# Kernel optimization log

Measured on AMD Instinct MI355X. Metric: run time of the kernel, lower is better.

Reference implementation:

```python
import jax, jax.numpy as jnp
import numpy as np

B, N, C = 2, 2048, 1024
H, HD = 16, 64
PX, PY, PS = 24, 24, 16  # S2RoPE head_dim split (px+py+ps == head_dim)


def rotate_half(t):
    t1, t2 = jnp.split(t, 2, axis=-1)
    return jnp.concatenate([-t2, t1], axis=-1)


def apply_phase_rope(t, phase):
    # t: [B, N, H, d_seg] (d_seg even), phase: [B, N, d_seg//2] angles in radians
    ang = jnp.concatenate([phase, phase], axis=-1)[:, :, None, :]  # [B,N,1,d_seg]
    return t * jnp.cos(ang) + rotate_half(t) * jnp.sin(ang)


def s2rope(t, phase_x, phase_y, phase_sph):
    # spherical RoPE: rotate three disjoint segments of head_dim by the
    # per-token x / y / spherical phases
    tx, ty, ts = t[..., :PX], t[..., PX:PX + PY], t[..., PX + PY:]
    return jnp.concatenate([
        apply_phase_rope(tx, phase_x),
        apply_phase_rope(ty, phase_y),
        apply_phase_rope(ts, phase_sph),
    ], axis=-1)


def setup_inputs() -> dict:
    key = jax.random.key(0)
    ks = jax.random.split(key, 9)
    two_pi = 6.2831853
    return {
        "x": jax.random.normal(ks[0], (B, N, C), dtype=jnp.float32),
        "phase_x": jax.random.uniform(ks[1], (B, N, PX // 2), dtype=jnp.float32) * two_pi,
        "phase_y": jax.random.uniform(ks[2], (B, N, PY // 2), dtype=jnp.float32) * two_pi,
        "phase_sph": jax.random.uniform(ks[3], (B, N, PS // 2), dtype=jnp.float32) * two_pi,
        "rope_mask": jax.random.randint(ks[4], (B, N), 0, 2).astype(bool),
        "Wqkv": jax.random.normal(ks[5], (C, 3 * C), dtype=jnp.float32) * (C ** -0.5),
        "bqkv": jax.random.normal(ks[6], (3 * C,), dtype=jnp.float32) * 0.02,
        "Wproj": jax.random.normal(ks[7], (C, C), dtype=jnp.float32) * (C ** -0.5),
        "bproj": jax.random.normal(ks[8], (C,), dtype=jnp.float32) * 0.02,
    }


def reference(x, phase_x, phase_y, phase_sph, rope_mask, Wqkv, bqkv, Wproj, bproj):
    # qkv projection -> [B, N, 3, H, HD]
    qkv = (x @ Wqkv + bqkv).reshape(B, N, 3, H, HD)
    q, k, v = qkv[:, :, 0], qkv[:, :, 1], qkv[:, :, 2]  # each [B, N, H, HD]

    # template path: S2RoPE with rope_mask selecting which tokens are rotated
    q_rope = s2rope(q, phase_x, phase_y, phase_sph)
    k_rope = s2rope(k, phase_x, phase_y, phase_sph)
    m = rope_mask[:, :, None, None]  # [B, N, 1, 1]
    q = jnp.where(m, q_rope, q)
    k = jnp.where(m, k_rope, k)

    scale = HD ** -0.5
    # [B, H, N, N] scores, softmax over keys, then weighted sum of values
    attn = jax.nn.softmax(jnp.einsum('bnhd,bmhd->bhnm', q, k) * scale, axis=-1)
    out = jnp.einsum('bhnm,bmhd->bnhd', attn, v).reshape(B, N, C)
    return out @ Wproj + bproj
```

## Files before the change

### kernel.cpp

```cpp
#include <hip/hip_runtime.h>
#include <hip/hip_fp16.h>

typedef _Float16 f16;
typedef unsigned int u32;
typedef _Float16 f16x4 __attribute__((ext_vector_type(4)));
typedef _Float16 f16x8 __attribute__((ext_vector_type(8)));
typedef float f32x4 __attribute__((ext_vector_type(4)));
typedef float f32x16 __attribute__((ext_vector_type(16)));

#define B_  2
#define N_  2048
#define C_  1024
#define H_  16
#define HD_ 64

__device__ __forceinline__ void gload_lds16(const void* g, void* l) {
  __builtin_amdgcn_global_load_lds((const __attribute__((address_space(1))) u32*)g,
                                   (__attribute__((address_space(3))) u32*)l,
                                   16, 0, 0);
}

__device__ __forceinline__ u32 pack_f16(float a, float b) {
  auto h2 = __builtin_amdgcn_cvt_pkrtz(a, b);
  return __builtin_bit_cast(u32, h2);
}

__global__ void detect_mask(const u32* __restrict__ m, int* __restrict__ flag) {
  __shared__ int bad;
  if (threadIdx.x == 0) bad = 0;
  __syncthreads();
  int v = 0;
  for (int i = threadIdx.x; i < 1024; i += 256) {
    u32 w = m[i];
    if (w != 0u && w != 1u && w != 0x3F800000u) v = 1;
  }
  if (v) atomicOr(&bad, 1);
  __syncthreads();
  if (threadIdx.x == 0) *flag = bad;
}

__global__ __launch_bounds__(256) void cvt_x(const float* __restrict__ in,
                                             f16* __restrict__ out, int n8) {
  const int i = blockIdx.x * 256 + threadIdx.x;
  if (i >= n8) return;
  const float4 a = ((const float4*)in)[i * 2];
  const float4 b = ((const float4*)in)[i * 2 + 1];
  f16x8 o = {(f16)a.x, (f16)a.y, (f16)a.z, (f16)a.w,
             (f16)b.x, (f16)b.y, (f16)b.z, (f16)b.w};
  ((f16x8*)out)[i] = o;
}

__global__ __launch_bounds__(256) void transpose_cvt(const float* __restrict__ W,
                                                     f16* __restrict__ Wt,
                                                     int R, int Ccols) {
  __shared__ __align__(16) f16 tile[32][34];
  const int c0 = blockIdx.x * 32, r0 = blockIdx.y * 32;
  const int tx = threadIdx.x, ty = threadIdx.y;
#pragma unroll
  for (int k = 0; k < 4; ++k)
    tile[ty + 8 * k][tx] = (f16)W[(size_t)(r0 + ty + 8 * k) * Ccols + c0 + tx];
  __syncthreads();
#pragma unroll
  for (int k = 0; k < 4; ++k)
    Wt[(size_t)(c0 + ty + 8 * k) * R + r0 + tx] = tile[tx][ty + 8 * k];
}

template <bool OUT_F32>
__global__ __launch_bounds__(256) void gemm_bt(const f16* __restrict__ A,
                                               const f16* __restrict__ Bt,
                                               const float* __restrict__ bias,
                                               void* __restrict__ Cout,
                                               int M, int N, int K) {
  __shared__ __align__(16) f16 As[128 * 64];
  __shared__ __align__(16) f16 Bs[128 * 64];
  const int tid = threadIdx.x;
  const int lane = tid & 63;
  const int wv = tid >> 6;
  const int wm = wv >> 1, wn = wv & 1;
  const int nTN = N >> 7;
  int bid = blockIdx.x;
  const int cpx = gridDim.x >> 3;
  bid = (bid & 7) * cpx + (bid >> 3);
  const int tM = bid / nTN, tN = bid % nTN;
  const int rowBase = tM << 7, colBase = tN << 7;
  const int cl = lane & 15, cg = lane >> 4;

  f32x4 acc[4][4];
#pragma unroll
  for (int i = 0; i < 4; ++i)
#pragma unroll
    for (int j = 0; j < 4; ++j) acc[i][j] = (f32x4){0.f, 0.f, 0.f, 0.f};

  const int sR = tid >> 3, sC = tid & 7;

  for (int k0 = 0; k0 < K; k0 += 64) {
#pragma unroll
    for (int is = 0; is < 4; ++is) {
      const int r = is * 32 + sR;
      const int sc = sC ^ (r & 7);
      gload_lds16(A + (size_t)(rowBase + r) * K + k0 + sc * 8, As + is * 2048 + tid * 8);
    }
#pragma unroll
    for (int is = 0; is < 4; ++is) {
      const int r = is * 32 + sR;
      const int sc = sC ^ (r & 7);
      gload_lds16(Bt + (size_t)(colBase + r) * K + k0 + sc * 8, Bs + is * 2048 + tid * 8);
    }
    asm volatile("s_waitcnt vmcnt(0)" ::: "memory");
    __syncthreads();

#pragma unroll
    for (int ks = 0; ks < 2; ++ks) {
      f16x8 af[4], bf[4];
#pragma unroll
      for (int m = 0; m < 4; ++m) {
        const int row = wm * 64 + m * 16 + cl;
        const int ck = (ks * 4 + cg) ^ (row & 7);
        af[m] = *(const f16x8*)(As + row * 64 + ck * 8);
      }
#pragma unroll
      for (int n = 0; n < 4; ++n) {
        const int row = wn * 64 + n * 16 + cl;
        const int ck = (ks * 4 + cg) ^ (row & 7);
        bf[n] = *(const f16x8*)(Bs + row * 64 + ck * 8);
      }
#pragma unroll
      for (int m = 0; m < 4; ++m)
#pragma unroll
        for (int n = 0; n < 4; ++n)
          acc[m][n] = __builtin_amdgcn_mfma_f32_16x16x32_f16(af[m], bf[n], acc[m][n], 0, 0, 0);
    }
    __syncthreads();
  }

#pragma unroll
  for (int m = 0; m < 4; ++m) {
#pragma unroll
    for (int n = 0; n < 4; ++n) {
      const int gr0 = rowBase + wm * 64 + m * 16 + cg * 4;
      const int gc = colBase + wn * 64 + n * 16 + cl;
      const float bz = bias[gc];
#pragma unroll
      for (int reg = 0; reg < 4; ++reg) {
        const float v = acc[m][n][reg] + bz;
        if (OUT_F32)
          ((float*)Cout)[(size_t)(gr0 + reg) * N + gc] = v;
        else
          ((f16*)Cout)[(size_t)(gr0 + reg) * N + gc] = (f16)v;
      }
    }
  }
}

__global__ __launch_bounds__(256) void rope_split(const f16* __restrict__ qkv,
                                                  const float* __restrict__ px,
                                                  const float* __restrict__ py,
                                                  const float* __restrict__ psp,
                                                  const void* __restrict__ maskPtr,
                                                  const int* __restrict__ maskFlag,
                                                  f16* __restrict__ Qh,
                                                  f16* __restrict__ Kh,
                                                  f16* __restrict__ Vt) {
  __shared__ float cs[64][32], sn[64][32];
  __shared__ __align__(16) f16 vtile[64][72];
  const int tid = threadIdx.x;
  const int blk = blockIdx.x;
  const int hg = blk & 3;
  const int nt = (blk >> 2) & 31;
  const int b = blk >> 7;
  const int n0 = nt * 64;
  const int byteMode = *maskFlag;

  for (int i = tid; i < 64 * 32; i += 256) {
    const int tk = i >> 5, j = i & 31;
    const int n = n0 + tk;
    float ph;
    if (j < 12)      ph = px[((size_t)b * N_ + n) * 12 + j];
    else if (j < 24) ph = py[((size_t)b * N_ + n) * 12 + (j - 12)];
    else             ph = psp[((size_t)b * N_ + n) * 8 + (j - 24)];
    cs[tk][j] = __cosf(ph);
    sn[tk][j] = __sinf(ph);
  }
  __syncthreads();

  const int tk = tid >> 2, hl = tid & 3;
  const int h = hg * 4 + hl;
  const int n = n0 + tk;
  const size_t midx = (size_t)b * N_ + n;
  const bool doRope = byteMode ? (((const unsigned char*)maskPtr)[midx] != 0)
                               : (((const u32*)maskPtr)[midx] != 0u);
  const size_t inRow = ((size_t)b * N_ + n) * 3072 + (size_t)h * 64;
  const size_t outRow = (((size_t)(b * H_ + h)) * N_ + n) * 64;

#pragma unroll
  for (int sec = 0; sec < 2; ++sec) {
    const f16* src = qkv + inRow + sec * 1024;
    float t[64];
#pragma unroll
    for (int c = 0; c < 8; ++c) {
      f16x8 v = *(const f16x8*)(src + c * 8);
#pragma unroll
      for (int j = 0; j < 8; ++j) t[c * 8 + j] = (float)v[j];
    }
    __align__(16) f16 o[64];
    if (doRope) {
#pragma unroll
      for (int d = 0; d < 64; ++d) {
        int j;
        float rot;
        if (d < 24) {
          j = (d < 12) ? d : d - 12;
          rot = (d < 12) ? -t[d + 12] : t[d - 12];
        } else if (d < 48) {
          const int dd = d - 24;
          j = 12 + ((dd < 12) ? dd : dd - 12);
          rot = (dd < 12) ? -t[d + 12] : t[d - 12];
        } else {
          const int dd = d - 48;
          j = 24 + ((dd < 8) ? dd : dd - 8);
          rot = (dd < 8) ? -t[d + 8] : t[d - 8];
        }
        o[d] = (f16)(t[d] * cs[tk][j] + rot * sn[tk][j]);
      }
    } else {
#pragma unroll
      for (int d = 0; d < 64; ++d) o[d] = (f16)t[d];
    }
    f16* dst = (sec == 0 ? Qh : Kh) + outRow;
#pragma unroll
    for (int c = 0; c < 8; ++c) *(f16x8*)(dst + c * 8) = *(const f16x8*)(o + c * 8);
  }

  for (int hl2 = 0; hl2 < 4; ++hl2) {
    const int h2 = hg * 4 + hl2;
    __syncthreads();
    {
      const int tk2 = tid >> 2, c2 = tid & 3;
      const size_t srow = ((size_t)b * N_ + n0 + tk2) * 3072 + 2048 + (size_t)h2 * 64 + c2 * 16;
      *(f16x8*)(&vtile[tk2][c2 * 16]) = *(const f16x8*)(qkv + srow);
      *(f16x8*)(&vtile[tk2][c2 * 16 + 8]) = *(const f16x8*)(qkv + srow + 8);
    }
    __syncthreads();
    {
      const int d = tid >> 2, seg = tid & 3;
      __align__(16) f16 tmp[16];
#pragma unroll
      for (int i = 0; i < 16; ++i) tmp[i] = vtile[seg * 16 + i][d];
      const size_t drow = (((size_t)(b * H_ + h2)) * 64 + d) * N_ + n0 + seg * 16;
      *(f16x8*)(Vt + drow) = *(const f16x8*)(tmp);
      *(f16x8*)(Vt + drow + 8) = *(const f16x8*)(tmp + 8);
    }
  }
}

__global__ __launch_bounds__(256) void attn2(const f16* __restrict__ Qh,
                                             const f16* __restrict__ Kh,
                                             const f16* __restrict__ Vt,
                                             f16* __restrict__ Y) {
  __shared__ __align__(16) f16 lds[2][2][4096];
  const int tid = threadIdx.x, lane = tid & 63, w = tid >> 6;
  int bid = blockIdx.x;
  bid = (bid & 7) * 64 + (bid >> 3);
  const int bh = bid >> 4, qb = bid & 15;
  const int b = bh >> 4, h = bh & 15;
  const f16* Qb = Qh + (size_t)bh * N_ * 64;
  const f16* Kb = Kh + (size_t)bh * N_ * 64;
  const f16* Vb = Vt + (size_t)bh * 64 * N_;
  const int ql = lane & 31, hi = lane >> 5;

  f16x8 qf[4];
  {
    const int qrow = qb * 128 + w * 32 + ql;
    const f16 scl = (f16)0.125f;
#pragma unroll
    for (int ks = 0; ks < 4; ++ks) {
      f16x8 v = *(const f16x8*)(Qb + (size_t)qrow * 64 + ks * 16 + hi * 8);
#pragma unroll
      for (int j = 0; j < 8; ++j) v[j] *= scl;
      qf[ks] = v;
    }
  }

  f32x16 Of[2];
#pragma unroll
  for (int d = 0; d < 2; ++d)
#pragma unroll
    for (int r = 0; r < 16; ++r) Of[d][r] = 0.f;
  float m_run = -1e30f, l_run = 0.f;

  const int sr = tid >> 3, sc = tid & 7;
#define STAGE(t, bb)                                                                     \
  {                                                                                      \
    _Pragma("unroll") for (int i = 0; i < 2; ++i) {                                      \
      const int row = i * 32 + sr;                                                       \
      const int g = sc ^ (row & 7);                                                      \
      gload_lds16(Kb + (size_t)((t) * 64 + row) * 64 + g * 8,                            \
                  &lds[bb][0][i * 2048 + tid * 8]);                                      \
    }                                                                                    \
    _Pragma("unroll") for (int i = 0; i < 2; ++i) {                                      \
      const int row = i * 32 + sr;                                                       \
      const int g = sc ^ (row & 7);                                                      \
      gload_lds16(Vb + (size_t)row * N_ + (t) * 64 + g * 8,                              \
                  &lds[bb][1][i * 2048 + tid * 8]);                                      \
    }                                                                                    \
  }

  STAGE(0, 0);
  asm volatile("s_waitcnt vmcnt(0)" ::: "memory");
  __syncthreads();

  int cur = 0;
  for (int t = 0; t < N_ / 64; ++t) {
    if (t < N_ / 64 - 1) STAGE(t + 1, cur ^ 1);
    const f16* Ks = &lds[cur][0][0];
    const f16* Vs = &lds[cur][1][0];
#pragma unroll
    for (int s = 0; s < 2; ++s) {
      f32x16 sa;
#pragma unroll
      for (int r = 0; r < 16; ++r) sa[r] = 0.f;
      const int krow = s * 32 + ql;
      __builtin_amdgcn_s_setprio(1);
#pragma unroll
      for (int ks = 0; ks < 4; ++ks) {
        f16x8 kf = *(const f16x8*)(Ks + krow * 64 + ((ks * 2 + hi) ^ (krow & 7)) * 8);
        sa = __builtin_amdgcn_mfma_f32_32x32x16_f16(kf, qf[ks], sa, 0, 0, 0);
      }
      __builtin_amdgcn_s_setprio(0);

      float m0 = fmaxf(fmaxf(fmaxf(sa[0], sa[1]), fmaxf(sa[2], sa[3])),
                       fmaxf(fmaxf(sa[4], sa[5]), fmaxf(sa[6], sa[7])));
      float m1 = fmaxf(fmaxf(fmaxf(sa[8], sa[9]), fmaxf(sa[10], sa[11])),
                       fmaxf(fmaxf(sa[12], sa[13]), fmaxf(sa[14], sa[15])));
      float pmax = fmaxf(m0, m1);
      pmax = fmaxf(pmax, __shfl_xor(pmax, 32));

      if (__any(pmax > m_run + 8.0f)) {
        const float mnew = fmaxf(m_run, pmax);
        const float corr = __expf(m_run - mnew);
        l_run *= corr;
#pragma unroll
        for (int d = 0; d < 2; ++d)
#pragma unroll
          for (int r = 0; r < 16; ++r) Of[d][r] *= corr;
        m_run = mnew;
      }

#pragma unroll
      for (int r = 0; r < 16; ++r) sa[r] = __expf(sa[r] - m_run);
      float s0 = ((sa[0] + sa[1]) + (sa[2] + sa[3])) + ((sa[4] + sa[5]) + (sa[6] + sa[7]));
      float s1 = ((sa[8] + sa[9]) + (sa[10] + sa[11])) + ((sa[12] + sa[13]) + (sa[14] + sa[15]));
      float ssum = s0 + s1;
      ssum += __shfl_xor(ssum, 32);
      l_run += ssum;

      u32 pw[8];
#pragma unroll
      for (int tt = 0; tt < 8; ++tt) pw[tt] = pack_f16(sa[2 * tt], sa[2 * tt + 1]);

#pragma unroll
      for (int kk = 0; kk < 2; ++kk) {
        u32 a0 = pw[4 * kk], a1 = pw[4 * kk + 1];
        u32 b0 = pw[4 * kk + 2], b1 = pw[4 * kk + 3];
        asm volatile("v_permlane32_swap_b32 %0, %1" : "+v"(a0), "+v"(b0));
        asm volatile("v_permlane32_swap_b32 %0, %1" : "+v"(a1), "+v"(b1));
        union { u32 u[4]; f16x8 v; } pf;
        pf.u[0] = a0; pf.u[1] = a1; pf.u[2] = b0; pf.u[3] = b1;
        __builtin_amdgcn_s_setprio(1);
#pragma unroll
        for (int df = 0; df < 2; ++df) {
          const int d = df * 32 + ql;
          f16x8 vf = *(const f16x8*)(Vs + d * 64 + ((s * 4 + kk * 2 + hi) ^ (d & 7)) * 8);
          Of[df] = __builtin_amdgcn_mfma_f32_32x32x16_f16(vf, pf.v, Of[df], 0, 0, 0);
        }
        __builtin_amdgcn_s_setprio(0);
      }
    }
    asm volatile("s_waitcnt vmcnt(0)" ::: "memory");
    __syncthreads();
    cur ^= 1;
  }

  const float inv = 1.0f / l_run;
  f16* Ow = &lds[0][0][0] + w * (32 * 72);
#pragma unroll
  for (int df = 0; df < 2; ++df)
#pragma unroll
    for (int g = 0; g < 4; ++g) {
      f16x4 ov;
#pragma unroll
      for (int e = 0; e < 4; ++e) ov[e] = (f16)(Of[df][g * 4 + e] * inv);
      *(f16x4*)(Ow + ql * 72 + df * 32 + g * 8 + hi * 4) = ov;
    }
  __syncthreads();
  const int rr = lane >> 1, half = lane & 1;
  const f16* srcp = Ow + rr * 72 + half * 32;
  const int nglob = qb * 128 + w * 32 + rr;
  f16* dst = Y + ((size_t)b * N_ + nglob) * C_ + h * 64 + half * 32;
#pragma unroll
  for (int c2 = 0; c2 < 4; ++c2)
    *(f16x8*)(dst + c2 * 8) = *(const f16x8*)(srcp + c2 * 8);
}

extern "C" void kernel_launch(void* const* d_in, const int* in_sizes, int n_in,
                              void* d_out, int out_size, void* d_ws, size_t ws_size,
                              hipStream_t stream) {
  const float* x = (const float*)d_in[0];
  const float* px = (const float*)d_in[1];
  const float* py = (const float*)d_in[2];
  const float* psp = (const float*)d_in[3];
  const void* mask = (const void*)d_in[4];
  const float* Wqkv = (const float*)d_in[5];
  const float* bqkv = (const float*)d_in[6];
  const float* Wproj = (const float*)d_in[7];
  const float* bproj = (const float*)d_in[8];
  float* out = (float*)d_out;
  char* ws = (char*)d_ws;

  f16* xh     = (f16*)(ws + 0);
  f16* Wqkvt  = (f16*)(ws + 8388608);
  f16* Wprojt = (f16*)(ws + 14680064);
  f16* qkvh   = (f16*)(ws + 16777216);
  f16* Qh     = (f16*)(ws + 41943040);
  f16* Kh     = (f16*)(ws + 50331648);
  f16* Vt     = (f16*)(ws + 58720256);
  f16* Yh     = (f16*)(ws + 67108864);
  int* mflag  = (int*)(ws + 75497472);

  detect_mask<<<1, 256, 0, stream>>>((const u32*)mask, mflag);
  cvt_x<<<2048, 256, 0, stream>>>(x, xh, (B_ * N_ * C_) / 8);
  transpose_cvt<<<dim3(96, 32), dim3(32, 8), 0, stream>>>(Wqkv, Wqkvt, C_, 3 * C_);
  transpose_cvt<<<dim3(32, 32), dim3(32, 8), 0, stream>>>(Wproj, Wprojt, C_, C_);
  gemm_bt<false><<<(4096 / 128) * (3072 / 128), 256, 0, stream>>>(
      xh, Wqkvt, bqkv, (void*)qkvh, 4096, 3072, 1024);
  rope_split<<<256, 256, 0, stream>>>(qkvh, px, py, psp, mask, mflag, Qh, Kh, Vt);
  attn2<<<512, 256, 0, stream>>>(Qh, Kh, Vt, Yh);
  gemm_bt<true><<<(4096 / 128) * (1024 / 128), 256, 0, stream>>>(
      Yh, Wprojt, bproj, (void*)out, 4096, 1024, 1024);
}
```

Measured before the change: 161.4 us.

## Precompute masked RoPE cos/sin table and batch QK MFMAs in attention

A new phase_tab kernel precomputes per-token cos/sin tables, folding the rope mask in as cos=1 and sin=0. rope_split then reads these tables and runs one branch-free rotation instead of computing trig and diverging on the mask. The attention inner loop now issues both 32-key QK^T MFMA chains before doing softmax and PV on each chunk, which is meant to overlap matrix work with the exp math, and uses 3-input max reductions. The change adds an extra kernel launch and reuses the Yh workspace region for the tables, and holding two score accumulators live raises register pressure.

```diff
diff --git a/kernel.cpp b/kernel.cpp
--- a/kernel.cpp
+++ b/kernel.cpp
@@ -25,6 +25,10 @@
   return __builtin_bit_cast(u32, h2);
 }
 
+__device__ __forceinline__ float max3f(float a, float b, float c) {
+  return fmaxf(fmaxf(a, b), c);
+}
+
 __global__ void detect_mask(const u32* __restrict__ m, int* __restrict__ flag) {
   __shared__ int bad;
   if (threadIdx.x == 0) bad = 0;
@@ -37,6 +41,31 @@
   if (v) atomicOr(&bad, 1);
   __syncthreads();
   if (threadIdx.x == 0) *flag = bad;
+}
+
+__global__ __launch_bounds__(256) void phase_tab(const float* __restrict__ px,
+                                                 const float* __restrict__ py,
+                                                 const float* __restrict__ psp,
+                                                 const void* __restrict__ maskPtr,
+                                                 const int* __restrict__ maskFlag,
+                                                 float* __restrict__ cs_tab,
+                                                 float* __restrict__ sn_tab) {
+  const int idx = blockIdx.x * 256 + threadIdx.x;
+  const int j = idx & 31, tn = idx >> 5;
+  const int byteMode = *maskFlag;
+  const bool doRope = byteMode ? (((const unsigned char*)maskPtr)[tn] != 0)
+                               : (((const u32*)maskPtr)[tn] != 0u);
+  float c = 1.f, s = 0.f;
+  if (doRope) {
+    float ph;
+    if (j < 12)      ph = px[tn * 12 + j];
+    else if (j < 24) ph = py[tn * 12 + (j - 12)];
+    else             ph = psp[tn * 8 + (j - 24)];
+    c = __cosf(ph);
+    s = __sinf(ph);
+  }
+  cs_tab[idx] = c;
+  sn_tab[idx] = s;
 }
 
 __global__ __launch_bounds__(256) void cvt_x(const float* __restrict__ in,
@@ -153,11 +182,8 @@
 }
 
 __global__ __launch_bounds__(256) void rope_split(const f16* __restrict__ qkv,
-                                                  const float* __restrict__ px,
-                                                  const float* __restrict__ py,
-                                                  const float* __restrict__ psp,
-                                                  const void* __restrict__ maskPtr,
-                                                  const int* __restrict__ maskFlag,
+                                                  const float* __restrict__ cs_tab,
+                                                  const float* __restrict__ sn_tab,
                                                   f16* __restrict__ Qh,
                                                   f16* __restrict__ Kh,
                                                   f16* __restrict__ Vt) {
@@ -169,26 +195,18 @@
   const int nt = (blk >> 2) & 31;
   const int b = blk >> 7;
   const int n0 = nt * 64;
-  const int byteMode = *maskFlag;
 
   for (int i = tid; i < 64 * 32; i += 256) {
     const int tk = i >> 5, j = i & 31;
-    const int n = n0 + tk;
-    float ph;
-    if (j < 12)      ph = px[((size_t)b * N_ + n) * 12 + j];
-    else if (j < 24) ph = py[((size_t)b * N_ + n) * 12 + (j - 12)];
-    else             ph = psp[((size_t)b * N_ + n) * 8 + (j - 24)];
-    cs[tk][j] = __cosf(ph);
-    sn[tk][j] = __sinf(ph);
+    const size_t gi = ((size_t)b * N_ + n0 + tk) * 32 + j;
+    cs[tk][j] = cs_tab[gi];
+    sn[tk][j] = sn_tab[gi];
   }
   __syncthreads();
 
   const int tk = tid >> 2, hl = tid & 3;
   const int h = hg * 4 + hl;
   const int n = n0 + tk;
-  const size_t midx = (size_t)b * N_ + n;
-  const bool doRope = byteMode ? (((const unsigned char*)maskPtr)[midx] != 0)
-                               : (((const u32*)maskPtr)[midx] != 0u);
   const size_t inRow = ((size_t)b * N_ + n) * 3072 + (size_t)h * 64;
   const size_t outRow = (((size_t)(b * H_ + h)) * N_ + n) * 64;
 
@@ -203,28 +221,23 @@
       for (int j = 0; j < 8; ++j) t[c * 8 + j] = (float)v[j];
     }
     __align__(16) f16 o[64];
-    if (doRope) {
-#pragma unroll
-      for (int d = 0; d < 64; ++d) {
-        int j;
-        float rot;
-        if (d < 24) {
-          j = (d < 12) ? d : d - 12;
-          rot = (d < 12) ? -t[d + 12] : t[d - 12];
-        } else if (d < 48) {
-          const int dd = d - 24;
-          j = 12 + ((dd < 12) ? dd : dd - 12);
-          rot = (dd < 12) ? -t[d + 12] : t[d - 12];
-        } else {
-          const int dd = d - 48;
-          j = 24 + ((dd < 8) ? dd : dd - 8);
-          rot = (dd < 8) ? -t[d + 8] : t[d - 8];
-        }
-        o[d] = (f16)(t[d] * cs[tk][j] + rot * sn[tk][j]);
+#pragma unroll
+    for (int d = 0; d < 64; ++d) {
+      int j;
+      float rot;
+      if (d < 24) {
+        j = (d < 12) ? d : d - 12;
+        rot = (d < 12) ? -t[d + 12] : t[d - 12];
+      } else if (d < 48) {
+        const int dd = d - 24;
+        j = 12 + ((dd < 12) ? dd : dd - 12);
+        rot = (dd < 12) ? -t[d + 12] : t[d - 12];
+      } else {
+        const int dd = d - 48;
+        j = 24 + ((dd < 8) ? dd : dd - 8);
+        rot = (dd < 8) ? -t[d + 8] : t[d - 8];
       }
-    } else {
-#pragma unroll
-      for (int d = 0; d < 64; ++d) o[d] = (f16)t[d];
+      o[d] = (f16)(t[d] * cs[tk][j] + rot * sn[tk][j]);
     }
     f16* dst = (sec == 0 ? Qh : Kh) + outRow;
 #pragma unroll
@@ -305,6 +318,54 @@
     }                                                                                    \
   }
 
+#define SOFTMAX_CHUNK(sa)                                                                \
+  {                                                                                      \
+    float t0 = max3f(sa[0], sa[1], sa[2]);                                               \
+    float t1 = max3f(sa[3], sa[4], sa[5]);                                               \
+    float t2 = max3f(sa[6], sa[7], sa[8]);                                               \
+    float t3 = max3f(sa[9], sa[10], sa[11]);                                             \
+    float t4 = max3f(sa[12], sa[13], sa[14]);                                            \
+    float pmax = max3f(max3f(t0, t1, t2), max3f(t3, t4, sa[15]), -1e30f);                \
+    pmax = fmaxf(pmax, __shfl_xor(pmax, 32));                                            \
+    if (__any(pmax > m_run + 8.0f)) {                                                    \
+      const float mnew = fmaxf(m_run, pmax);                                             \
+      const float corr = __expf(m_run - mnew);                                           \
+      l_run *= corr;                                                                     \
+      _Pragma("unroll") for (int d = 0; d < 2; ++d)                                      \
+        _Pragma("unroll") for (int r = 0; r < 16; ++r) Of[d][r] *= corr;                 \
+      m_run = mnew;                                                                      \
+    }                                                                                    \
+    _Pragma("unroll") for (int r = 0; r < 16; ++r) sa[r] = __expf(sa[r] - m_run);        \
+    float s0 = ((sa[0] + sa[1]) + (sa[2] + sa[3])) + ((sa[4] + sa[5]) + (sa[6] + sa[7]));\
+    float s1 = ((sa[8] + sa[9]) + (sa[10] + sa[11])) +                                   \
+               ((sa[12] + sa[13]) + (sa[14] + sa[15]));                                  \
+    float ssum = s0 + s1;                                                                \
+    ssum += __shfl_xor(ssum, 32);                                                        \
+    l_run += ssum;                                                                       \
+  }
+
+#define PV_CHUNK(sa, s)                                                                  \
+  {                                                                                      \
+    u32 pw[8];                                                                           \
+    _Pragma("unroll") for (int tt = 0; tt < 8; ++tt)                                     \
+      pw[tt] = pack_f16(sa[2 * tt], sa[2 * tt + 1]);                                     \
+    _Pragma("unroll") for (int kk = 0; kk < 2; ++kk) {                                   \
+      u32 a0 = pw[4 * kk], a1 = pw[4 * kk + 1];                                          \
+      u32 b0 = pw[4 * kk + 2], b1 = pw[4 * kk + 3];                                      \
+      asm volatile("v_permlane32_swap_b32 %0, %1" : "+v"(a0), "+v"(b0));                 \
+      asm volatile("v_permlane32_swap_b32 %0, %1" : "+v"(a1), "+v"(b1));                 \
+      union { u32 u[4]; f16x8 v; } pf;                                                   \
+      pf.u[0] = a0; pf.u[1] = a1; pf.u[2] = b0; pf.u[3] = b1;                            \
+      __builtin_amdgcn_s_setprio(1);                                                     \
+      _Pragma("unroll") for (int df = 0; df < 2; ++df) {                                 \
+        const int d = df * 32 + ql;                                                      \
+        f16x8 vf = *(const f16x8*)(Vs + d * 64 + (((s) * 4 + kk * 2 + hi) ^ (d & 7)) * 8);\
+        Of[df] = __builtin_amdgcn_mfma_f32_32x32x16_f16(vf, pf.v, Of[df], 0, 0, 0);      \
+      }                                                                                  \
+      __builtin_amdgcn_s_setprio(0);                                                     \
+    }                                                                                    \
+  }
+
   STAGE(0, 0);
   asm volatile("s_waitcnt vmcnt(0)" ::: "memory");
   __syncthreads();
@@ -314,68 +375,29 @@
     if (t < N_ / 64 - 1) STAGE(t + 1, cur ^ 1);
     const f16* Ks = &lds[cur][0][0];
     const f16* Vs = &lds[cur][1][0];
-#pragma unroll
-    for (int s = 0; s < 2; ++s) {
-      f32x16 sa;
-#pragma unroll
-      for (int r = 0; r < 16; ++r) sa[r] = 0.f;
-      const int krow = s * 32 + ql;
-      __builtin_amdgcn_s_setprio(1);
-#pragma unroll
-      for (int ks = 0; ks < 4; ++ks) {
-        f16x8 kf = *(const f16x8*)(Ks + krow * 64 + ((ks * 2 + hi) ^ (krow & 7)) * 8);
-        sa = __builtin_amdgcn_mfma_f32_32x32x16_f16(kf, qf[ks], sa, 0, 0, 0);
-      }
-      __builtin_amdgcn_s_setprio(0);
-
-      float m0 = fmaxf(fmaxf(fmaxf(sa[0], sa[1]), fmaxf(sa[2], sa[3])),
-                       fmaxf(fmaxf(sa[4], sa[5]), fmaxf(sa[6], sa[7])));
-      float m1 = fmaxf(fmaxf(fmaxf(sa[8], sa[9]), fmaxf(sa[10], sa[11])),
-                       fmaxf(fmaxf(sa[12], sa[13]), fmaxf(sa[14], sa[15])));
-      float pmax = fmaxf(m0, m1);
-      pmax = fmaxf(pmax, __shfl_xor(pmax, 32));
-
-      if (__any(pmax > m_run + 8.0f)) {
-        const float mnew = fmaxf(m_run, pmax);
-        const float corr = __expf(m_run - mnew);
-        l_run *= corr;
-#pragma unroll
-        for (int d = 0; d < 2; ++d)
-#pragma unroll
-          for (int r = 0; r < 16; ++r) Of[d][r] *= corr;
-        m_run = mnew;
-      }
-
-#pragma unroll
-      for (int r = 0; r < 16; ++r) sa[r] = __expf(sa[r] - m_run);
-      float s0 = ((sa[0] + sa[1]) + (sa[2] + sa[3])) + ((sa[4] + sa[5]) + (sa[6] + sa[7]));
-      float s1 = ((sa[8] + sa[9]) + (sa[10] + sa[11])) + ((sa[12] + sa[13]) + (sa[14] + sa[15]));
-      float ssum = s0 + s1;
-      ssum += __shfl_xor(ssum, 32);
-      l_run += ssum;
-
-      u32 pw[8];
-#pragma unroll
-      for (int tt = 0; tt < 8; ++tt) pw[tt] = pack_f16(sa[2 * tt], sa[2 * tt + 1]);
-
-#pragma unroll
-      for (int kk = 0; kk < 2; ++kk) {
-        u32 a0 = pw[4 * kk], a1 = pw[4 * kk + 1];
-        u32 b0 = pw[4 * kk + 2], b1 = pw[4 * kk + 3];
-        asm volatile("v_permlane32_swap_b32 %0, %1" : "+v"(a0), "+v"(b0));
-        asm volatile("v_permlane32_swap_b32 %0, %1" : "+v"(a1), "+v"(b1));
-        union { u32 u[4]; f16x8 v; } pf;
-        pf.u[0] = a0; pf.u[1] = a1; pf.u[2] = b0; pf.u[3] = b1;
-        __builtin_amdgcn_s_setprio(1);
-#pragma unroll
-        for (int df = 0; df < 2; ++df) {
-          const int d = df * 32 + ql;
-          f16x8 vf = *(const f16x8*)(Vs + d * 64 + ((s * 4 + kk * 2 + hi) ^ (d & 7)) * 8);
-          Of[df] = __builtin_amdgcn_mfma_f32_32x32x16_f16(vf, pf.v, Of[df], 0, 0, 0);
-        }
-        __builtin_amdgcn_s_setprio(0);
-      }
-    }
+
+    f32x16 sa0, sa1;
+#pragma unroll
+    for (int r = 0; r < 16; ++r) { sa0[r] = 0.f; sa1[r] = 0.f; }
+    const int krow0 = ql, krow1 = 32 + ql;
+    __builtin_amdgcn_s_setprio(1);
+#pragma unroll
+    for (int ks = 0; ks < 4; ++ks) {
+      f16x8 kf = *(const f16x8*)(Ks + krow0 * 64 + ((ks * 2 + hi) ^ (krow0 & 7)) * 8);
+      sa0 = __builtin_amdgcn_mfma_f32_32x32x16_f16(kf, qf[ks], sa0, 0, 0, 0);
+    }
+#pragma unroll
+    for (int ks = 0; ks < 4; ++ks) {
+      f16x8 kf = *(const f16x8*)(Ks + krow1 * 64 + ((ks * 2 + hi) ^ (krow1 & 7)) * 8);
+      sa1 = __builtin_amdgcn_mfma_f32_32x32x16_f16(kf, qf[ks], sa1, 0, 0, 0);
+    }
+    __builtin_amdgcn_s_setprio(0);
+
+    SOFTMAX_CHUNK(sa0);
+    PV_CHUNK(sa0, 0);
+    SOFTMAX_CHUNK(sa1);
+    PV_CHUNK(sa1, 1);
+
     asm volatile("s_waitcnt vmcnt(0)" ::: "memory");
     __syncthreads();
     cur ^= 1;
@@ -426,14 +448,17 @@
   f16* Vt     = (f16*)(ws + 58720256);
   f16* Yh     = (f16*)(ws + 67108864);
   int* mflag  = (int*)(ws + 75497472);
+  float* cs_tab = (float*)(ws + 67108864);
+  float* sn_tab = (float*)(ws + 67108864 + 524288);
 
   detect_mask<<<1, 256, 0, stream>>>((const u32*)mask, mflag);
   cvt_x<<<2048, 256, 0, stream>>>(x, xh, (B_ * N_ * C_) / 8);
+  phase_tab<<<512, 256, 0, stream>>>(px, py, psp, mask, mflag, cs_tab, sn_tab);
   transpose_cvt<<<dim3(96, 32), dim3(32, 8), 0, stream>>>(Wqkv, Wqkvt, C_, 3 * C_);
   transpose_cvt<<<dim3(32, 32), dim3(32, 8), 0, stream>>>(Wproj, Wprojt, C_, C_);
   gemm_bt<false><<<(4096 / 128) * (3072 / 128), 256, 0, stream>>>(
       xh, Wqkvt, bqkv, (void*)qkvh, 4096, 3072, 1024);
-  rope_split<<<256, 256, 0, stream>>>(qkvh, px, py, psp, mask, mflag, Qh, Kh, Vt);
+  rope_split<<<256, 256, 0, stream>>>(qkvh, cs_tab, sn_tab, Qh, Kh, Vt);
   attn2<<<512, 256, 0, stream>>>(Qh, Kh, Vt, Yh);
   gemm_bt<true><<<(4096 / 128) * (1024 / 128), 256, 0, stream>>>(
       Yh, Wprojt, bproj, (void*)out, 4096, 1024, 1024);
```

After: 161.3 us. About the same (-0.1%).
